# Optimization experiments

Hardware: AMD Instinct MI355X
Metric: run time of the kernel (lower is better)

The kernel has to match this reference:

```python
import jax, jax.numpy as jnp
import numpy as np

B, C, H, W = 64, 64, 112, 112   # batch, features(channels), spatial
HID = 256                        # hidden_size
T = 4                            # time_steps
BN_EPS = 1e-5


@jax.custom_vjp
def heaviside(x, th):
    # SpikeFunction.forward: (x >= th).float()
    return (x >= th).astype(x.dtype)

def _hv_fwd(x, th):
    return heaviside(x, th), (x, th)

def _hv_bwd(res, g):
    x, th = res
    # surrogate: clamp(1 - |x - th|, 0) with gamma = 1.0; no grad to threshold
    surr = jnp.clip(1.0 - jnp.abs(x - th), 0.0, None)
    return (g * surr, jnp.zeros_like(th))

heaviside.defvjp(_hv_fwd, _hv_bwd)


def setup_inputs() -> dict:
    key = jax.random.key(0)
    ks = jax.random.split(key, 6)
    x = jax.random.normal(ks[0], (B, C, H, W), jnp.float32)
    w_in = jax.random.normal(ks[1], (HID, C), jnp.float32) * 0.05       # input_proj (no bias)
    w_out = jax.random.normal(ks[2], (C, HID), jnp.float32) * 0.05      # output_proj (no bias)
    conv_w = jax.random.normal(ks[3], (C, 1, 3, 3), jnp.float32) * 0.1  # depthwise conv, groups=C
    bn1_gamma = jnp.ones((HID,), jnp.float32)
    bn1_beta = jnp.zeros((HID,), jnp.float32)
    bn1_mean = jnp.zeros((HID,), jnp.float32)
    bn1_var = jnp.ones((HID,), jnp.float32)
    bn2_gamma = jnp.ones((C,), jnp.float32)
    bn2_beta = jnp.zeros((C,), jnp.float32)
    bn2_mean = jnp.zeros((C,), jnp.float32)
    bn2_var = jnp.ones((C,), jnp.float32)
    decay_param = jnp.asarray(np.log(0.85 / 0.15), jnp.float32)  # logit(decay_init=0.85)
    v_th = jnp.asarray(0.5, jnp.float32)
    scale = jnp.full((C,), 0.5, jnp.float32)
    return {
        "x": x, "w_in": w_in, "bn1_gamma": bn1_gamma, "bn1_beta": bn1_beta,
        "bn1_mean": bn1_mean, "bn1_var": bn1_var, "decay_param": decay_param,
        "v_th": v_th, "w_out": w_out, "conv_w": conv_w,
        "bn2_gamma": bn2_gamma, "bn2_beta": bn2_beta, "bn2_mean": bn2_mean,
        "bn2_var": bn2_var, "scale": scale,
    }


def reference(x, w_in, bn1_gamma, bn1_beta, bn1_mean, bn1_var, decay_param,
              v_th, w_out, conv_w, bn2_gamma, bn2_beta, bn2_mean, bn2_var, scale):
    b = x.shape[0]
    # global average pool -> (b, C)
    x_feat = jnp.mean(x, axis=(2, 3))
    # input projection + BatchNorm1d (eval, running stats) + ReLU
    h_vec = x_feat @ w_in.T                                   # (b, HID)
    h_vec = (h_vec - bn1_mean) * jax.lax.rsqrt(bn1_var + BN_EPS) * bn1_gamma + bn1_beta
    h_vec = jax.nn.relu(h_vec)

    # PLIF recurrence over T steps (single layer); states detached between steps
    d = jax.nn.sigmoid(decay_param)
    mem_s = jnp.zeros_like(h_vec)
    sp_s = jnp.zeros_like(h_vec)
    final_spike = sp_s
    for _ in range(T):
        mem = d * (mem_s - v_th * sp_s) + h_vec
        denom = jnp.mean(jnp.abs(mem), axis=1, keepdims=True) + 1e-6  # per-sample norm
        mem = mem / denom
        spike = heaviside(mem, v_th)
        mem_s = jax.lax.stop_gradient(mem)
        sp_s = jax.lax.stop_gradient(spike)
        final_spike = spike

    binary = 2.0 * final_spike - 1.0
    binary = binary @ w_out.T                                 # hidden != features -> project (b, C)
    mod_map = 1.0 + jnp.tanh(scale[None, :] * binary) * 0.5   # (b, C)

    # broadcast to spatial map (b, C, H, W)
    spatial = jnp.broadcast_to(mod_map[:, :, None, None], (b, C, H, W))

    # spatial refine: depthwise 3x3 conv + BN2d (eval) + ReLU
    y = jax.lax.conv_general_dilated(
        spatial, conv_w, window_strides=(1, 1), padding=((1, 1), (1, 1)),
        dimension_numbers=("NCHW", "OIHW", "NCHW"), feature_group_count=C)
    y = (y - bn2_mean[None, :, None, None]) * jax.lax.rsqrt(bn2_var + BN_EPS)[None, :, None, None]
    y = y * bn2_gamma[None, :, None, None] + bn2_beta[None, :, None, None]
    y = jax.nn.relu(y)
    return 1.0 + 0.25 * jnp.tanh(y)
```

## Files before the change

kernel.cpp:

```cpp
#include <hip/hip_runtime.h>
#include <math.h>

#define BB   64
#define CC   64
#define HH   112
#define WW   112
#define HIDN 256
#define PLANE   (HH * WW)
#define PLANE4  (PLANE / 4)
#define BODY4   3072
#define ROW4    (WW / 4)

typedef float fvec4 __attribute__((ext_vector_type(4)));

__global__ __launch_bounds__(256) void pool_kernel(const float* __restrict__ x,
                                                   float* __restrict__ xfeat) {
    int plane = blockIdx.x;
    const fvec4* p = (const fvec4*)(x + (size_t)plane * PLANE);
    int t = threadIdx.x;
    float s0 = 0.f, s1 = 0.f, s2 = 0.f, s3 = 0.f;
    #pragma unroll
    for (int i = t; i < BODY4; i += 256) {
        fvec4 v = p[i];
        s0 += v.x; s1 += v.y; s2 += v.z; s3 += v.w;
    }
    if (t < PLANE4 - BODY4) {
        fvec4 v = p[BODY4 + t];
        s0 += v.x; s1 += v.y; s2 += v.z; s3 += v.w;
    }
    float s = (s0 + s1) + (s2 + s3);
    for (int off = 32; off > 0; off >>= 1) s += __shfl_down(s, off, 64);
    __shared__ float red[4];
    int lane = t & 63, wid = t >> 6;
    if (lane == 0) red[wid] = s;
    __syncthreads();
    if (t == 0) {
        float tt = (red[0] + red[1]) + (red[2] + red[3]);
        xfeat[plane] = tt / (float)PLANE;
    }
}

__global__ __launch_bounds__(256) void plif_kernel(
        const float* __restrict__ xfeat,
        const float* __restrict__ w_in,
        const float* __restrict__ bn1_gamma, const float* __restrict__ bn1_beta,
        const float* __restrict__ bn1_mean,  const float* __restrict__ bn1_var,
        const float* __restrict__ decay_param, const float* __restrict__ v_th,
        const float* __restrict__ w_out, const float* __restrict__ conv_w,
        const float* __restrict__ bn2_gamma, const float* __restrict__ bn2_beta,
        const float* __restrict__ bn2_mean,  const float* __restrict__ bn2_var,
        const float* __restrict__ scale,
        float* __restrict__ vals) {
    int b = blockIdx.x;
    int h = threadIdx.x;
    __shared__ float  xf[CC];
    __shared__ double red[4];
    __shared__ float  sbin[HIDN];
    __shared__ double bmred[CC][4];
    __shared__ double modv[CC];

    if (h < CC) xf[h] = xfeat[b * CC + h];
    __syncthreads();

    double hv = 0.0;
    #pragma unroll 8
    for (int c = 0; c < CC; ++c)
        hv += (double)xf[c] * (double)w_in[h * CC + c];

    hv = (hv - (double)bn1_mean[h]) / sqrt((double)bn1_var[h] + 1e-5)
             * (double)bn1_gamma[h] + (double)bn1_beta[h];
    if (hv < 0.0) hv = 0.0;

    double d   = 1.0 / (1.0 + exp(-(double)decay_param[0]));
    double vth = (double)v_th[0];

    double mem_s = 0.0, sp_s = 0.0, spike = 0.0;
    int lane = h & 63, wid = h >> 6;
    for (int t = 0; t < 4; ++t) {
        double mem = d * (mem_s - vth * sp_s) + hv;
        double a = fabs(mem);
        for (int off = 32; off > 0; off >>= 1) a += __shfl_down(a, off, 64);
        if (lane == 0) red[wid] = a;
        __syncthreads();
        double denom = ((red[0] + red[1]) + (red[2] + red[3])) / (double)HIDN + 1e-6;
        __syncthreads();
        mem = mem / denom;
        spike = (mem >= vth) ? 1.0 : 0.0;
        mem_s = mem;
        sp_s  = spike;
    }

    sbin[h] = (float)(2.0 * spike - 1.0);
    __syncthreads();

    {
        int c = h & 63, part = h >> 6;
        const float* wr = w_out + c * HIDN + part * 64;
        const float* sb = sbin + part * 64;
        double bm = 0.0;
        #pragma unroll 8
        for (int k = 0; k < 64; ++k)
            bm += (double)sb[k] * (double)wr[k];
        bmred[c][part] = bm;
    }
    __syncthreads();
    if (h < CC) {
        double t = ((bmred[h][0] + bmred[h][1]) + bmred[h][2]) + bmred[h][3];
        modv[h] = 1.0 + tanh((double)scale[h] * t) * 0.5;
    }
    __syncthreads();

    for (int task = h; task < CC * 9; task += 256) {
        int c  = task / 9;
        int cl = task - c * 9;
        int rc = cl / 3, cc2 = cl - rc * 3;
        int kh0 = (rc == 0) ? 1 : 0, kh1 = (rc == 2) ? 1 : 2;
        int kw0 = (cc2 == 0) ? 1 : 0, kw1 = (cc2 == 2) ? 1 : 2;
        double S = 0.0;
        for (int kh = kh0; kh <= kh1; ++kh)
            for (int kw = kw0; kw <= kw1; ++kw)
                S += (double)conv_w[c * 9 + kh * 3 + kw];
        double y = modv[c] * S;
        y = (y - (double)bn2_mean[c]) / sqrt((double)bn2_var[c] + 1e-5)
                * (double)bn2_gamma[c] + (double)bn2_beta[c];
        if (y < 0.0) y = 0.0;
        vals[(b * CC + c) * 9 + cl] = (float)(1.0 + 0.25 * tanh(y));
    }
}

__global__ __launch_bounds__(256) void fill_kernel(const float* __restrict__ vals,
                                                   float* __restrict__ out) {
    int plane = blockIdx.x;
    __shared__ float v[9];
    if (threadIdx.x < 9) v[threadIdx.x] = vals[plane * 9 + threadIdx.x];
    __syncthreads();
    fvec4* o4 = (fvec4*)(out + (size_t)plane * PLANE);
    for (int i = threadIdx.x; i < PLANE4; i += 256) {
        int r = i / ROW4;
        int q = i - r * ROW4;
        int base = (r == 0) ? 0 : ((r == HH - 1) ? 6 : 3);
        float m = v[base + 1];
        fvec4 val = { (q == 0) ? v[base] : m, m, m,
                      (q == ROW4 - 1) ? v[base + 2] : m };
        __builtin_nontemporal_store(val, &o4[i]);
    }
}

extern "C" void kernel_launch(void* const* d_in, const int* in_sizes, int n_in,
                              void* d_out, int out_size, void* d_ws, size_t ws_size,
                              hipStream_t stream) {
    const float* x          = (const float*)d_in[0];
    const float* w_in       = (const float*)d_in[1];
    const float* bn1_gamma  = (const float*)d_in[2];
    const float* bn1_beta   = (const float*)d_in[3];
    const float* bn1_mean   = (const float*)d_in[4];
    const float* bn1_var    = (const float*)d_in[5];
    const float* decay_p    = (const float*)d_in[6];
    const float* v_th       = (const float*)d_in[7];
    const float* w_out      = (const float*)d_in[8];
    const float* conv_w     = (const float*)d_in[9];
    const float* bn2_gamma  = (const float*)d_in[10];
    const float* bn2_beta   = (const float*)d_in[11];
    const float* bn2_mean   = (const float*)d_in[12];
    const float* bn2_var    = (const float*)d_in[13];
    const float* scale      = (const float*)d_in[14];
    float* out = (float*)d_out;

    float* xfeat = (float*)d_ws;
    float* vals  = xfeat + BB * CC;

    pool_kernel<<<BB * CC, 256, 0, stream>>>(x, xfeat);
    plif_kernel<<<BB, 256, 0, stream>>>(xfeat, w_in, bn1_gamma, bn1_beta,
                                        bn1_mean, bn1_var, decay_p, v_th,
                                        w_out, conv_w, bn2_gamma, bn2_beta,
                                        bn2_mean, bn2_var, scale, vals);
    fill_kernel<<<BB * CC, 256, 0, stream>>>(vals, out);
}
```

Before: 87.50 us.

## Fuse PLIF computation into fill kernel, recomputing per-sample state per plane

Merges the per-sample PLIF/projection kernel with the output fill kernel so that each plane's block computes its own 9 boundary values before writing. This removes one kernel launch and the intermediate vals buffer. In exchange, the hidden-layer matvec and spiking iterations are recomputed redundantly for every channel of a sample, which adds double-precision work and latency before each block's stores.

```diff
diff --git a/kernel.cpp b/kernel.cpp
--- a/kernel.cpp
+++ b/kernel.cpp
@@ -40,7 +40,7 @@
     }
 }
 
-__global__ __launch_bounds__(256) void plif_kernel(
+__global__ __launch_bounds__(256) void plif_fill_kernel(
         const float* __restrict__ xfeat,
         const float* __restrict__ w_in,
         const float* __restrict__ bn1_gamma, const float* __restrict__ bn1_beta,
@@ -50,22 +50,26 @@
         const float* __restrict__ bn2_gamma, const float* __restrict__ bn2_beta,
         const float* __restrict__ bn2_mean,  const float* __restrict__ bn2_var,
         const float* __restrict__ scale,
-        float* __restrict__ vals) {
-    int b = blockIdx.x;
-    int h = threadIdx.x;
+        float* __restrict__ out) {
+    const int plane = blockIdx.x;
+    const int b = plane >> 6;
+    const int c = plane & 63;
+    const int h = threadIdx.x;
+
     __shared__ float  xf[CC];
-    __shared__ double red[4];
+    __shared__ double redd[4];
     __shared__ float  sbin[HIDN];
-    __shared__ double bmred[CC][4];
-    __shared__ double modv[CC];
+    __shared__ double bmp[4];
+    __shared__ double modv_s;
+    __shared__ float  v[9];
 
     if (h < CC) xf[h] = xfeat[b * CC + h];
     __syncthreads();
 
     double hv = 0.0;
     #pragma unroll 8
-    for (int c = 0; c < CC; ++c)
-        hv += (double)xf[c] * (double)w_in[h * CC + c];
+    for (int cc2 = 0; cc2 < CC; ++cc2)
+        hv += (double)xf[cc2] * (double)w_in[h * CC + cc2];
 
     hv = (hv - (double)bn1_mean[h]) / sqrt((double)bn1_var[h] + 1e-5)
              * (double)bn1_gamma[h] + (double)bn1_beta[h];
@@ -80,9 +84,9 @@
         double mem = d * (mem_s - vth * sp_s) + hv;
         double a = fabs(mem);
         for (int off = 32; off > 0; off >>= 1) a += __shfl_down(a, off, 64);
-        if (lane == 0) red[wid] = a;
+        if (lane == 0) redd[wid] = a;
         __syncthreads();
-        double denom = ((red[0] + red[1]) + (red[2] + red[3])) / (double)HIDN + 1e-6;
+        double denom = ((redd[0] + redd[1]) + (redd[2] + redd[3])) / (double)HIDN + 1e-6;
         __syncthreads();
         mem = mem / denom;
         spike = (mem >= vth) ? 1.0 : 0.0;
@@ -93,49 +97,40 @@
     sbin[h] = (float)(2.0 * spike - 1.0);
     __syncthreads();
 
-    {
-        int c = h & 63, part = h >> 6;
-        const float* wr = w_out + c * HIDN + part * 64;
-        const float* sb = sbin + part * 64;
+    if (h < 4) {
+        const float* wr = w_out + c * HIDN + h * 64;
+        const float* sb = sbin + h * 64;
         double bm = 0.0;
         #pragma unroll 8
         for (int k = 0; k < 64; ++k)
             bm += (double)sb[k] * (double)wr[k];
-        bmred[c][part] = bm;
+        bmp[h] = bm;
     }
     __syncthreads();
-    if (h < CC) {
-        double t = ((bmred[h][0] + bmred[h][1]) + bmred[h][2]) + bmred[h][3];
-        modv[h] = 1.0 + tanh((double)scale[h] * t) * 0.5;
+    if (h == 0) {
+        double t = ((bmp[0] + bmp[1]) + bmp[2]) + bmp[3];
+        modv_s = 1.0 + tanh((double)scale[c] * t) * 0.5;
     }
     __syncthreads();
 
-    for (int task = h; task < CC * 9; task += 256) {
-        int c  = task / 9;
-        int cl = task - c * 9;
-        int rc = cl / 3, cc2 = cl - rc * 3;
+    if (h < 9) {
+        int rc = h / 3, cc2 = h - rc * 3;
         int kh0 = (rc == 0) ? 1 : 0, kh1 = (rc == 2) ? 1 : 2;
         int kw0 = (cc2 == 0) ? 1 : 0, kw1 = (cc2 == 2) ? 1 : 2;
         double S = 0.0;
         for (int kh = kh0; kh <= kh1; ++kh)
             for (int kw = kw0; kw <= kw1; ++kw)
                 S += (double)conv_w[c * 9 + kh * 3 + kw];
-        double y = modv[c] * S;
+        double y = modv_s * S;
         y = (y - (double)bn2_mean[c]) / sqrt((double)bn2_var[c] + 1e-5)
                 * (double)bn2_gamma[c] + (double)bn2_beta[c];
         if (y < 0.0) y = 0.0;
-        vals[(b * CC + c) * 9 + cl] = (float)(1.0 + 0.25 * tanh(y));
+        v[h] = (float)(1.0 + 0.25 * tanh(y));
     }
-}
+    __syncthreads();
 
-__global__ __launch_bounds__(256) void fill_kernel(const float* __restrict__ vals,
-                                                   float* __restrict__ out) {
-    int plane = blockIdx.x;
-    __shared__ float v[9];
-    if (threadIdx.x < 9) v[threadIdx.x] = vals[plane * 9 + threadIdx.x];
-    __syncthreads();
     fvec4* o4 = (fvec4*)(out + (size_t)plane * PLANE);
-    for (int i = threadIdx.x; i < PLANE4; i += 256) {
+    for (int i = h; i < PLANE4; i += 256) {
         int r = i / ROW4;
         int q = i - r * ROW4;
         int base = (r == 0) ? 0 : ((r == HH - 1) ? 6 : 3);
@@ -167,12 +162,9 @@
     float* out = (float*)d_out;
 
     float* xfeat = (float*)d_ws;
-    float* vals  = xfeat + BB * CC;
 
     pool_kernel<<<BB * CC, 256, 0, stream>>>(x, xfeat);
-    plif_kernel<<<BB, 256, 0, stream>>>(xfeat, w_in, bn1_gamma, bn1_beta,
-                                        bn1_mean, bn1_var, decay_p, v_th,
-                                        w_out, conv_w, bn2_gamma, bn2_beta,
-                                        bn2_mean, bn2_var, scale, vals);
-    fill_kernel<<<BB * CC, 256, 0, stream>>>(vals, out);
+    plif_fill_kernel<<<BB * CC, 256, 0, stream>>>(
+        xfeat, w_in, bn1_gamma, bn1_beta, bn1_mean, bn1_var, decay_p, v_th,
+        w_out, conv_w, bn2_gamma, bn2_beta, bn2_mean, bn2_var, scale, out);
 }
```

After: 98.67 us. 1.13x slower.
